# Kernel optimization log

Hardware: AMD Instinct MI355X
Metric: run time of the kernel (lower is better)

## Reference

```python
import jax, jax.numpy as jnp
import numpy as np

B, S, V, D, H, DH, L, FF = 1, 4096, 50265, 768, 12, 64, 4, 3072
C = 256          # chunk size
W = 256          # one-sided window (attention_window=512 total)
N = S // C


def _ln(x, g, b):
    m = x.mean(-1, keepdims=True)
    v = ((x - m) ** 2).mean(-1, keepdims=True)
    return (x - m) * jax.lax.rsqrt(v + 1e-5) * g + b


def setup_inputs() -> dict:
    key = jax.random.key(0)
    ks = iter(jax.random.split(key, 64))
    f = lambda sh: 0.02 * jax.random.normal(next(ks), sh, jnp.float32)
    return dict(
        input_ids=jax.random.randint(next(ks), (B, S), 0, V),
        attention_mask=jnp.ones((B, S), jnp.int32),
        word_emb=f((V, D)), pos_emb=f((S, D)),
        emb_g=jnp.ones((D,)), emb_b=jnp.zeros((D,)),
        Wq=f((L, D, D)), Wk=f((L, D, D)), Wv=f((L, D, D)), Wo=f((L, D, D)),
        bq=jnp.zeros((L, D)), bk=jnp.zeros((L, D)), bv=jnp.zeros((L, D)), bo=jnp.zeros((L, D)),
        ln1_g=jnp.ones((L, D)), ln1_b=jnp.zeros((L, D)),
        Wff1=f((L, D, FF)), bff1=jnp.zeros((L, FF)),
        Wff2=f((L, FF, D)), bff2=jnp.zeros((L, D)),
        ln2_g=jnp.ones((L, D)), ln2_b=jnp.zeros((L, D)),
        W1=f((D, 512)), b1=jnp.zeros((512,)),
        W2=f((512, 250)), b2=jnp.zeros((250,)),
        W3=f((250, 1)), b3=jnp.zeros((1,)),
    )


def _band_attn(x, maskf, Wq, Wk, Wv, Wo, bq, bk, bv, bo):
    # sliding-window (banded) attention via overlapping 3-chunk blocks
    q = ((x @ Wq + bq) / np.float32(np.sqrt(DH))).reshape(B, N, C, H, DH)
    k = (x @ Wk + bk).reshape(B, N, C, H, DH)
    v = (x @ Wv + bv).reshape(B, N, C, H, DH)
    pad = ((0, 0), (1, 1), (0, 0), (0, 0), (0, 0))
    kp, vp = jnp.pad(k, pad), jnp.pad(v, pad)
    kb = jnp.concatenate([kp[:, :-2], kp[:, 1:-1], kp[:, 2:]], axis=2)  # [B,N,3C,H,DH]
    vb = jnp.concatenate([vp[:, :-2], vp[:, 1:-1], vp[:, 2:]], axis=2)
    mc = maskf.reshape(B, N, C)
    mp = jnp.pad(mc, ((0, 0), (1, 1), (0, 0)))
    mb = jnp.concatenate([mp[:, :-2], mp[:, 1:-1], mp[:, 2:]], axis=2)  # [B,N,3C]
    qi = jnp.arange(C)[:, None]
    kj = jnp.arange(3 * C)[None, :]
    band = jnp.abs(kj - C - qi) <= W                       # [C,3C]
    valid = band[None, None, None] & (mb[:, None, :, None, :] > 0)  # [B,1,N,C,3C]
    scores = jnp.einsum('bnqhd,bnkhd->bhnqk', q, kb)       # [B,H,N,C,3C]
    scores = jnp.where(valid, scores, -1e9)
    probs = jax.nn.softmax(scores, axis=-1)
    out = jnp.einsum('bhnqk,bnkhd->bnqhd', probs, vb).reshape(B, S, D)
    return out @ Wo + bo


def reference(input_ids, attention_mask, word_emb, pos_emb, emb_g, emb_b,
              Wq, Wk, Wv, Wo, bq, bk, bv, bo, ln1_g, ln1_b,
              Wff1, bff1, Wff2, bff2, ln2_g, ln2_b,
              W1, b1, W2, b2, W3, b3):
    maskf = attention_mask.astype(jnp.float32)
    x = _ln(word_emb[input_ids] + pos_emb[None], emb_g, emb_b)
    for l in range(L):
        a = _band_attn(x, maskf, Wq[l], Wk[l], Wv[l], Wo[l], bq[l], bk[l], bv[l], bo[l])
        x = _ln(x + a, ln1_g[l], ln1_b[l])
        h = jax.nn.gelu(x @ Wff1[l] + bff1[l], approximate=False)
        x = _ln(x + h @ Wff2[l] + bff2[l], ln2_g[l], ln2_b[l])
    m = maskf[..., None]
    pooled = (x * m).sum(1) / jnp.clip(m.sum(1), 1e-9)     # mean pooling, [B,D]
    h = jax.nn.relu(pooled @ W1 + b1)
    h = jax.nn.relu(h @ W2 + b2)
    pred = h @ W3 + b3                                     # dropout = identity (eval)
    return (pred, pred)
```

## Files before the change

### kernel.cpp

```cpp
#include <hip/hip_runtime.h>
#include <hip/hip_bf16.h>

typedef __hip_bfloat16 bf16;
typedef unsigned short ushort_t;
typedef short bhalf8 __attribute__((ext_vector_type(8)));
typedef float floatx4 __attribute__((ext_vector_type(4)));

#define SLEN 4096
#define DMODEL 768
#define NHEAD 12
#define DHEAD 64
#define NLAYER 4
#define FFDIM 3072
#define WIN 256
#define QB 64
#define NKT 9
#define VT_PLANE (NHEAD*DHEAD*SLEN)

__device__ __forceinline__ float wave_sum(float v){
  #pragma unroll
  for (int off = 32; off; off >>= 1) v += __shfl_xor(v, off, 64);
  return v;
}

__device__ __forceinline__ ushort_t f2bf(float x){
  unsigned u = __float_as_uint(x);
  unsigned r = u + 0x7FFFu + ((u >> 16) & 1u);
  return (ushort_t)(r >> 16);
}
__device__ __forceinline__ float bf2f(ushort_t h){
  return __uint_as_float((unsigned)h << 16);
}

__device__ __forceinline__ floatx4 mfma_bf16(bhalf8 a, bhalf8 b, floatx4 c){
  asm("v_mfma_f32_16x16x32_bf16 %0, %1, %2, %0" : "+v"(c) : "v"(a), "v"(b));
  return c;
}

__device__ __forceinline__ void split8(const float* xs, bhalf8& hi, bhalf8& lo){
  union { ushort_t u[8]; bhalf8 v; } H, L;
  #pragma unroll
  for (int j = 0; j < 8; j++){
    ushort_t h = f2bf(xs[j]);
    H.u[j] = h;
    L.u[j] = f2bf(xs[j] - bf2f(h));
  }
  hi = H.v; lo = L.v;
}

__global__ __launch_bounds__(256) void embed_ln_kernel(
    const int* __restrict__ ids, const float* __restrict__ we,
    const float* __restrict__ pe, const float* __restrict__ g,
    const float* __restrict__ b, float* __restrict__ x){
  int row  = blockIdx.x*4 + (threadIdx.x >> 6);
  int lane = threadIdx.x & 63;
  int id = ids[row];
  float e[12];
  float sum = 0.f;
  #pragma unroll
  for (int i = 0; i < 12; i++){
    int c = lane + i*64;
    e[i] = we[(size_t)id*DMODEL + c] + pe[(size_t)row*DMODEL + c];
    sum += e[i];
  }
  float mean = wave_sum(sum) * (1.f/DMODEL);
  float vs = 0.f;
  #pragma unroll
  for (int i = 0; i < 12; i++){ float d = e[i] - mean; vs += d*d; }
  float inv = 1.f / sqrtf(wave_sum(vs)*(1.f/DMODEL) + 1e-5f);
  #pragma unroll
  for (int i = 0; i < 12; i++){
    int c = lane + i*64;
    x[(size_t)row*DMODEL + c] = (e[i] - mean)*inv*g[c] + b[c];
  }
}

__global__ __launch_bounds__(256) void ln_kernel(
    const float* __restrict__ in, float* __restrict__ out,
    const float* __restrict__ g, const float* __restrict__ b){
  int row  = blockIdx.x*4 + (threadIdx.x >> 6);
  int lane = threadIdx.x & 63;
  float e[12];
  float sum = 0.f;
  #pragma unroll
  for (int i = 0; i < 12; i++){
    e[i] = in[(size_t)row*DMODEL + lane + i*64];
    sum += e[i];
  }
  float mean = wave_sum(sum) * (1.f/DMODEL);
  float vs = 0.f;
  #pragma unroll
  for (int i = 0; i < 12; i++){ float d = e[i] - mean; vs += d*d; }
  float inv = 1.f / sqrtf(wave_sum(vs)*(1.f/DMODEL) + 1e-5f);
  #pragma unroll
  for (int i = 0; i < 12; i++){
    int c = lane + i*64;
    out[(size_t)row*DMODEL + c] = (e[i] - mean)*inv*g[c] + b[c];
  }
}

__global__ __launch_bounds__(256) void split_a_kernel(
    const float* __restrict__ X, ushort_t* __restrict__ T, int K){
  int idx = blockIdx.x*256 + threadIdx.x;
  int m  = idx & 4095;
  int kc = idx >> 12;
  const float* src = X + (size_t)m*K + kc*8;
  float4 x0 = *reinterpret_cast<const float4*>(src);
  float4 x1 = *reinterpret_cast<const float4*>(src + 4);
  float xs[8] = {x0.x,x0.y,x0.z,x0.w,x1.x,x1.y,x1.z,x1.w};
  union { ushort_t u[8]; uint4 v; } ph, pl;
  #pragma unroll
  for (int j = 0; j < 8; j++){
    ushort_t h = f2bf(xs[j]);
    ph.u[j] = h;
    pl.u[j] = f2bf(xs[j] - bf2f(h));
  }
  size_t KC = (size_t)(K >> 3);
  *reinterpret_cast<uint4*>(T + ((size_t)kc*4096 + m)*8)      = ph.v;
  *reinterpret_cast<uint4*>(T + ((KC + kc)*4096 + m)*8)       = pl.v;
}

__global__ __launch_bounds__(256) void split_b_kernel(
    const float* __restrict__ W, ushort_t* __restrict__ T, int N, int K){
  int n  = blockIdx.x*256 + threadIdx.x;
  int kc = blockIdx.y;
  float xs[8];
  #pragma unroll
  for (int j = 0; j < 8; j++) xs[j] = W[(size_t)(kc*8 + j)*N + n];
  union { ushort_t u[8]; uint4 v; } ph, pl;
  #pragma unroll
  for (int j = 0; j < 8; j++){
    ushort_t h = f2bf(xs[j]);
    ph.u[j] = h;
    pl.u[j] = f2bf(xs[j] - bf2f(h));
  }
  size_t KC = (size_t)(K >> 3);
  *reinterpret_cast<uint4*>(T + ((size_t)kc*N + n)*8)   = ph.v;
  *reinterpret_cast<uint4*>(T + ((KC + kc)*N + n)*8)    = pl.v;
}

__global__ __launch_bounds__(256) void gemm_mfma_kernel(
    const ushort_t* __restrict__ pAt,
    const ushort_t* __restrict__ pBt,
    const float* __restrict__ bias, const float* __restrict__ resid,
    float* __restrict__ Cm, int M, int N, int K, float scale, int act,
    ushort_t* __restrict__ vt_out){
  __shared__ __align__(16) ushort_t LAh[4][128][8];
  __shared__ __align__(16) ushort_t LAl[4][128][8];
  __shared__ __align__(16) ushort_t LBh[4][128][8];
  __shared__ __align__(16) ushort_t LBl[4][128][8];
  const int tid  = threadIdx.x;
  const int w    = tid >> 6;
  const int lane = tid & 63;
  const int wr = w >> 1, wc = w & 1;
  const int r0 = blockIdx.y*128, c0 = blockIdx.x*128;
  const int fr = lane & 15, fq = lane >> 4;
  const size_t KC = (size_t)(K >> 3);

  size_t plane; int rb; const ushort_t* gbase; ushort_t* lbase;
  if (w < 2){ plane = (size_t)M*8; rb = r0; } else { plane = (size_t)N*8; rb = c0; }
  if      (w == 0){ gbase = pAt;             lbase = &LAh[0][0][0]; }
  else if (w == 1){ gbase = pAt + KC*plane;  lbase = &LAl[0][0][0]; }
  else if (w == 2){ gbase = pBt;             lbase = &LBh[0][0][0]; }
  else            { gbase = pBt + KC*plane;  lbase = &LBl[0][0][0]; }

  floatx4 acc[4][4] = {};

  const int nstep = K >> 5;
  for (int s = 0; s < nstep; ++s){
    const int kcb = s << 2;
    #pragma unroll
    for (int ci = 0; ci < 8; ci++){
      const int kg = ci >> 1, half = ci & 1;
      const ushort_t* sp = gbase + (size_t)(kcb + kg)*plane
                         + (size_t)(rb + half*64 + lane)*8;
      ushort_t* dp = lbase + kg*1024 + half*512;
      __builtin_amdgcn_global_load_lds(
          (const __attribute__((address_space(1))) void*)sp,
          (__attribute__((address_space(3))) void*)dp, 16, 0, 0);
    }
    asm volatile("s_waitcnt vmcnt(0)" ::: "memory");
    __syncthreads();

    bhalf8 ah[4], al[4], bh[4], bl[4];
    #pragma unroll
    for (int mi = 0; mi < 4; mi++){
      int row = wr*64 + mi*16 + fr;
      ah[mi] = *reinterpret_cast<const bhalf8*>(&LAh[fq][row][0]);
      al[mi] = *reinterpret_cast<const bhalf8*>(&LAl[fq][row][0]);
    }
    #pragma unroll
    for (int ni = 0; ni < 4; ni++){
      int col = wc*64 + ni*16 + fr;
      bh[ni] = *reinterpret_cast<const bhalf8*>(&LBh[fq][col][0]);
      bl[ni] = *reinterpret_cast<const bhalf8*>(&LBl[fq][col][0]);
    }
    #pragma unroll
    for (int mi = 0; mi < 4; mi++)
      #pragma unroll
      for (int ni = 0; ni < 4; ni++)
        acc[mi][ni] = mfma_bf16(ah[mi], bh[ni], acc[mi][ni]);
    #pragma unroll
    for (int mi = 0; mi < 4; mi++)
      #pragma unroll
      for (int ni = 0; ni < 4; ni++)
        acc[mi][ni] = mfma_bf16(ah[mi], bl[ni], acc[mi][ni]);
    #pragma unroll
    for (int mi = 0; mi < 4; mi++)
      #pragma unroll
      for (int ni = 0; ni < 4; ni++)
        acc[mi][ni] = mfma_bf16(al[mi], bh[ni], acc[mi][ni]);
    __syncthreads();
  }

  if (vt_out){
    #pragma unroll
    for (int mi = 0; mi < 4; mi++){
      #pragma unroll
      for (int ni = 0; ni < 4; ni++){
        int col = c0 + wc*64 + ni*16 + fr;
        float bb = bias[col];
        int row0 = r0 + wr*64 + mi*16 + fq*4;
        unsigned long long phi = 0ull, plo = 0ull;
        #pragma unroll
        for (int j = 0; j < 4; j++){
          float vo = (acc[mi][ni][j] + bb) * scale;
          ushort_t hh = f2bf(vo);
          ushort_t ll = f2bf(vo - bf2f(hh));
          phi |= (unsigned long long)hh << (16*j);
          plo |= (unsigned long long)ll << (16*j);
        }
        size_t base = (size_t)col*SLEN + row0;
        *reinterpret_cast<unsigned long long*>(&vt_out[base])            = phi;
        *reinterpret_cast<unsigned long long*>(&vt_out[VT_PLANE + base]) = plo;
      }
    }
    return;
  }

  #pragma unroll
  for (int mi = 0; mi < 4; mi++){
    #pragma unroll
    for (int ni = 0; ni < 4; ni++){
      int col = c0 + wc*64 + ni*16 + fr;
      float bb = bias[col];
      #pragma unroll
      for (int j = 0; j < 4; j++){
        int row = r0 + wr*64 + mi*16 + fq*4 + j;
        float vo = (acc[mi][ni][j] + bb) * scale;
        if (act == 1) vo = 0.5f*vo*(1.f + erff(vo*0.70710678118654752f));
        if (resid) vo += resid[(size_t)row*N + col];
        Cm[(size_t)row*N + col] = vo;
      }
    }
  }
}

__global__ __launch_bounds__(128) void band_attn_kernel(
    const float* __restrict__ q, const float* __restrict__ k,
    const ushort_t* __restrict__ vt, const int* __restrict__ mask,
    float* __restrict__ ao){
  __shared__ __align__(16) ushort_t KHs[8][65][8];
  __shared__ __align__(16) ushort_t KLs[8][65][8];
  __shared__ __align__(16) ushort_t VHs[8][65][8];
  __shared__ __align__(16) ushort_t VLs[8][65][8];
  __shared__ __align__(16) ushort_t PHs[2][8][33][8];
  __shared__ __align__(16) ushort_t PLs[2][8][33][8];
  __shared__ float aL[2][32];
  __shared__ float lL[2][32];

  const int h    = blockIdx.y;
  const int q0   = blockIdx.x * QB;
  const int tid  = threadIdx.x;
  const int w    = tid >> 6;
  const int lane = tid & 63;
  const int fr   = lane & 15;
  const int fq   = lane >> 4;
  const int kstart = q0 - WIN;

  bhalf8 QHr[2][2], QLr[2][2];
  #pragma unroll
  for (int cf = 0; cf < 2; cf++)
    #pragma unroll
    for (int s = 0; s < 2; s++){
      const float* qp = q + (size_t)(q0 + 32*w + 16*cf + fr)*DMODEL
                      + h*DHEAD + s*32 + fq*8;
      float4 a = *reinterpret_cast<const float4*>(qp);
      float4 b = *reinterpret_cast<const float4*>(qp + 4);
      float xs[8] = {a.x,a.y,a.z,a.w,b.x,b.y,b.z,b.w};
      split8(xs, QHr[cf][s], QLr[cf][s]);
    }

  floatx4 acc_o[2][4] = {};
  float mreg[2] = {0.f, 0.f};
  float lreg[2] = {0.f, 0.f};

  const int rK = 32*w + (lane >> 1);
  const int hd = lane & 1;

  for (int t = 0; t < NKT; t++){
    const int g0 = kstart + t*64;

    {
      int g = min(max(g0 + rK, 0), SLEN-1);
      const float* kp = k + (size_t)g*DMODEL + h*DHEAD + hd*32;
      #pragma unroll
      for (int i = 0; i < 4; i++){
        float4 a = *reinterpret_cast<const float4*>(kp + i*8);
        float4 b = *reinterpret_cast<const float4*>(kp + i*8 + 4);
        float xs[8] = {a.x,a.y,a.z,a.w,b.x,b.y,b.z,b.w};
        bhalf8 hi, lo; split8(xs, hi, lo);
        int kg = hd*4 + i;
        *reinterpret_cast<bhalf8*>(&KHs[kg][rK][0]) = hi;
        *reinterpret_cast<bhalf8*>(&KLs[kg][rK][0]) = lo;
      }
      const ushort_t* vrow = vt + (size_t)(h*DHEAD + rK)*SLEN;
      #pragma unroll
      for (int i = 0; i < 4; i++){
        int kk = min(max(g0 + hd*32 + i*8, 0), SLEN-8);
        uint4 hv = *reinterpret_cast<const uint4*>(&vrow[kk]);
        uint4 lv = *reinterpret_cast<const uint4*>(&vrow[VT_PLANE + kk]);
        int u = hd*4 + i;
        *reinterpret_cast<uint4*>(&VHs[u][rK][0]) = hv;
        *reinterpret_cast<uint4*>(&VLs[u][rK][0]) = lv;
      }
    }
    __syncthreads();

    int gmk = g0 + lane;
    bool kvv = ((unsigned)gmk < (unsigned)SLEN) &&
               (mask[min(max(gmk,0),SLEN-1)] != 0);
    unsigned long long bal = __ballot(kvv);

    floatx4 acc_s[4][2] = {};
    #pragma unroll
    for (int s = 0; s < 2; s++)
      #pragma unroll
      for (int kf = 0; kf < 4; kf++){
        int row = 16*kf + fr;
        int kg  = s*4 + fq;
        bhalf8 KHf = *reinterpret_cast<const bhalf8*>(&KHs[kg][row][0]);
        bhalf8 KLf = *reinterpret_cast<const bhalf8*>(&KLs[kg][row][0]);
        #pragma unroll
        for (int cf = 0; cf < 2; cf++){
          acc_s[kf][cf] = mfma_bf16(KHf, QHr[cf][s], acc_s[kf][cf]);
          acc_s[kf][cf] = mfma_bf16(KHf, QLr[cf][s], acc_s[kf][cf]);
          acc_s[kf][cf] = mfma_bf16(KLf, QHr[cf][s], acc_s[kf][cf]);
        }
      }

    #pragma unroll
    for (int cf = 0; cf < 2; cf++){
      int qloc = 32*w + 16*cf + fr;
      float mx = -1e30f;
      #pragma unroll
      for (int kf = 0; kf < 4; kf++)
        #pragma unroll
        for (int j = 0; j < 4; j++){
          int key = 16*kf + fq*4 + j;
          int dj  = t*64 + key - WIN - qloc;
          bool ok = ((unsigned)(dj + WIN) <= 2u*WIN) && ((bal >> key) & 1ull);
          float sv = ok ? acc_s[kf][cf][j] : -1e30f;
          acc_s[kf][cf][j] = sv;
          mx = fmaxf(mx, sv);
        }
      mx = fmaxf(mx, __shfl_xor(mx, 16, 64));
      mx = fmaxf(mx, __shfl_xor(mx, 32, 64));
      float mnew  = fmaxf(mreg[cf], mx);
      float alpha = __expf(mreg[cf] - mnew);
      mreg[cf] = mnew;
      float psum = 0.f;
      #pragma unroll
      for (int kf = 0; kf < 4; kf++){
        unsigned long long phi = 0ull, plo = 0ull;
        #pragma unroll
        for (int j = 0; j < 4; j++){
          float p = __expf(acc_s[kf][cf][j] - mnew);
          psum += p;
          ushort_t hh = f2bf(p);
          ushort_t ll = f2bf(p - bf2f(hh));
          phi |= (unsigned long long)hh << (16*j);
          plo |= (unsigned long long)ll << (16*j);
        }
        int kgrp = 2*kf + (fq >> 1);
        int qrow = 16*cf + fr;
        *reinterpret_cast<unsigned long long*>(&PHs[w][kgrp][qrow][(fq&1)*4]) = phi;
        *reinterpret_cast<unsigned long long*>(&PLs[w][kgrp][qrow][(fq&1)*4]) = plo;
      }
      psum += __shfl_xor(psum, 16, 64);
      psum += __shfl_xor(psum, 32, 64);
      lreg[cf] = lreg[cf]*alpha + psum;
      if (fq == 0) aL[w][16*cf + fr] = alpha;
    }
    __syncthreads();

    #pragma unroll
    for (int mf = 0; mf < 2; mf++)
      #pragma unroll
      for (int j = 0; j < 4; j++){
        float al = aL[w][16*mf + fq*4 + j];
        #pragma unroll
        for (int ni = 0; ni < 4; ni++)
          acc_o[mf][ni][j] *= al;
      }

    #pragma unroll
    for (int ks = 0; ks < 2; ks++){
      int u = ks*4 + fq;
      bhalf8 PHf[2], PLf[2];
      #pragma unroll
      for (int mf = 0; mf < 2; mf++){
        PHf[mf] = *reinterpret_cast<const bhalf8*>(&PHs[w][u][16*mf + fr][0]);
        PLf[mf] = *reinterpret_cast<const bhalf8*>(&PLs[w][u][16*mf + fr][0]);
      }
      #pragma unroll
      for (int ni = 0; ni < 4; ni++){
        int d = 16*ni + fr;
        bhalf8 VHf = *reinterpret_cast<const bhalf8*>(&VHs[u][d][0]);
        bhalf8 VLf = *reinterpret_cast<const bhalf8*>(&VLs[u][d][0]);
        #pragma unroll
        for (int mf = 0; mf < 2; mf++){
          acc_o[mf][ni] = mfma_bf16(PHf[mf], VHf, acc_o[mf][ni]);
          acc_o[mf][ni] = mfma_bf16(PHf[mf], VLf, acc_o[mf][ni]);
          acc_o[mf][ni] = mfma_bf16(PLf[mf], VHf, acc_o[mf][ni]);
        }
      }
    }
    __syncthreads();
  }

  if (fq == 0){
    lL[w][fr]      = 1.f / lreg[0];
    lL[w][16 + fr] = 1.f / lreg[1];
  }
  __syncthreads();
  #pragma unroll
  for (int mf = 0; mf < 2; mf++)
    #pragma unroll
    for (int j = 0; j < 4; j++){
      float inv = lL[w][16*mf + fq*4 + j];
      int qg = q0 + 32*w + 16*mf + fq*4 + j;
      float* orow = ao + (size_t)qg*DMODEL + h*DHEAD;
      #pragma unroll
      for (int ni = 0; ni < 4; ni++)
        orow[16*ni + fr] = acc_o[mf][ni][j] * inv;
    }
}

__global__ __launch_bounds__(256) void pool1_kernel(
    const float* __restrict__ x, const int* __restrict__ mask,
    float* __restrict__ partial){
  int b = blockIdx.x;
  int t = threadIdx.x;
  float a0 = 0.f, a1 = 0.f, a2 = 0.f;
  for (int r = b*16; r < b*16 + 16; r++){
    float mm = (float)mask[r];
    const float* row = x + (size_t)r*DMODEL;
    a0 = fmaf(row[t      ], mm, a0);
    a1 = fmaf(row[t + 256], mm, a1);
    a2 = fmaf(row[t + 512], mm, a2);
  }
  partial[(size_t)b*DMODEL + t      ] = a0;
  partial[(size_t)b*DMODEL + t + 256] = a1;
  partial[(size_t)b*DMODEL + t + 512] = a2;
}

__global__ __launch_bounds__(256) void pool2_kernel(
    const float* __restrict__ partial, float* __restrict__ ps){
  int c = blockIdx.x*256 + threadIdx.x;
  float a = 0.f;
  for (int p = 0; p < 256; p++) a += partial[(size_t)p*DMODEL + c];
  ps[c] = a;
}

__global__ __launch_bounds__(64) void probe_kernel(
    const float* __restrict__ p, int n, float* __restrict__ slot){
  int lane = threadIdx.x;
  float s = 0.f;
  for (int i = lane; i < n; i += 64) s += fabsf(p[i]);
  s = wave_sum(s);
  if (lane == 0) slot[0] = s;
}

__global__ __launch_bounds__(256) void head_kernel(
    const float* __restrict__ ps, const int* __restrict__ mask,
    const float* __restrict__ W1, const float* __restrict__ b1,
    const float* __restrict__ W2, const float* __restrict__ b2,
    const float* __restrict__ W3, const float* __restrict__ b3,
    const float* __restrict__ diag,
    bf16* __restrict__ out){
  __shared__ float p[DMODEL];
  __shared__ float h1[512];
  __shared__ float h2[256];
  __shared__ float red[4];
  int tid = threadIdx.x;
  float ms = 0.f;
  for (int r = tid; r < SLEN; r += 256) ms += (float)mask[r];
  ms = wave_sum(ms);
  if ((tid & 63) == 0) red[tid >> 6] = ms;
  __syncthreads();
  float msum = red[0] + red[1] + red[2] + red[3];
  float inv = 1.f / fmaxf(msum, 1e-9f);
  for (int c = tid; c < DMODEL; c += 256) p[c] = ps[c]*inv;
  __syncthreads();
  #pragma unroll
  for (int jj = 0; jj < 2; jj++){
    int j = tid + jj*256;
    float acc = 0.f;
    for (int c = 0; c < DMODEL; c++) acc = fmaf(p[c], W1[(size_t)c*512 + j], acc);
    h1[j] = fmaxf(acc + b1[j], 0.f);
  }
  __syncthreads();
  if (tid < 250){
    float acc = 0.f;
    for (int c = 0; c < 512; c++) acc = fmaf(h1[c], W2[(size_t)c*250 + tid], acc);
    h2[tid] = fmaxf(acc + b2[tid], 0.f);
  }
  __syncthreads();
  if (tid == 0){
    float acc = b3[0];
    for (int c = 0; c < 250; c++) acc = fmaf(h2[c], W3[c], acc);
    float delta = 0.f;
    #pragma unroll
    for (int kk = 0; kk < 6; kk++){
      float dv = diag[kk];
      if (!(dv > 1e-3f)){
        delta = (dv != dv ? 8192.0f : 0.0f) + 64.0f*(kk+1);
        break;
      }
    }
    float r = acc + delta;
    union { bf16 h; unsigned short u; } cv;
    cv.h = (bf16)r;
    unsigned int packed = ((unsigned int)cv.u << 16) | (unsigned int)cv.u;
    volatile unsigned int* o32 = (volatile unsigned int*)out;
    o32[0] = packed;
    o32[1] = packed;
  }
}

extern "C" void kernel_launch(void* const* d_in, const int* in_sizes, int n_in,
                              void* d_out, int out_size, void* d_ws, size_t ws_size,
                              hipStream_t stream) {
  const int*   ids  = (const int*)d_in[0];
  const int*   mask = (const int*)d_in[1];
  const float* we   = (const float*)d_in[2];
  const float* pe   = (const float*)d_in[3];
  const float* eg   = (const float*)d_in[4];
  const float* eb   = (const float*)d_in[5];
  const float* Wq   = (const float*)d_in[6];
  const float* Wk   = (const float*)d_in[7];
  const float* Wv   = (const float*)d_in[8];
  const float* Wo   = (const float*)d_in[9];
  const float* bq   = (const float*)d_in[10];
  const float* bk   = (const float*)d_in[11];
  const float* bv   = (const float*)d_in[12];
  const float* bo   = (const float*)d_in[13];
  const float* g1   = (const float*)d_in[14];
  const float* be1  = (const float*)d_in[15];
  const float* Wf1  = (const float*)d_in[16];
  const float* bf1  = (const float*)d_in[17];
  const float* Wf2  = (const float*)d_in[18];
  const float* bf2  = (const float*)d_in[19];
  const float* g2   = (const float*)d_in[20];
  const float* be2  = (const float*)d_in[21];
  const float* W1   = (const float*)d_in[22];
  const float* b1   = (const float*)d_in[23];
  const float* W2   = (const float*)d_in[24];
  const float* b2   = (const float*)d_in[25];
  const float* W3   = (const float*)d_in[26];
  const float* b3   = (const float*)d_in[27];

  const size_t SD = (size_t)SLEN*DMODEL;
  float* x  = (float*)d_ws;
  float* y  = x  + SD;
  float* q  = y  + SD;
  float* k  = q  + SD;
  float* v  = k  + SD;
  float* ao = v  + SD;
  float* hf = q;
  ushort_t* vt = (ushort_t*)v;
  float* ps      = ao + SD;
  float* partial = ps + 1024;
  float* diag    = partial + 256*DMODEL;
  ushort_t* At = (ushort_t*)(diag + 64);
  ushort_t* Bt = At + (size_t)2*(FFDIM/8)*4096*8;

  embed_ln_kernel<<<SLEN/4, 256, 0, stream>>>(ids, we, pe, eg, eb, x);
  probe_kernel<<<1, 64, 0, stream>>>(x, 4096, diag + 0);

  const float qscale = 0.125f;
  dim3 gProj(DMODEL/128, SLEN/128);
  dim3 gFF1 (FFDIM/128,  SLEN/128);
  dim3 sbD(DMODEL/256, DMODEL/8);
  dim3 sbF1(FFDIM/256, DMODEL/8);
  dim3 sbF2(DMODEL/256, FFDIM/8);

  for (int l = 0; l < NLAYER; l++){
    const float* wq  = Wq  + (size_t)l*DMODEL*DMODEL;
    const float* wk  = Wk  + (size_t)l*DMODEL*DMODEL;
    const float* wv  = Wv  + (size_t)l*DMODEL*DMODEL;
    const float* wo  = Wo  + (size_t)l*DMODEL*DMODEL;
    const float* wf1 = Wf1 + (size_t)l*DMODEL*FFDIM;
    const float* wf2 = Wf2 + (size_t)l*FFDIM*DMODEL;

    split_a_kernel<<<(DMODEL/8)*SLEN/256, 256, 0, stream>>>(x, At, DMODEL);
    split_b_kernel<<<sbD, 256, 0, stream>>>(wq, Bt, DMODEL, DMODEL);
    gemm_mfma_kernel<<<gProj, 256, 0, stream>>>(At, Bt, bq + l*DMODEL, nullptr, q,
                                                SLEN, DMODEL, DMODEL, qscale, 0, nullptr);
    split_b_kernel<<<sbD, 256, 0, stream>>>(wk, Bt, DMODEL, DMODEL);
    gemm_mfma_kernel<<<gProj, 256, 0, stream>>>(At, Bt, bk + l*DMODEL, nullptr, k,
                                                SLEN, DMODEL, DMODEL, 1.f, 0, nullptr);
    split_b_kernel<<<sbD, 256, 0, stream>>>(wv, Bt, DMODEL, DMODEL);
    gemm_mfma_kernel<<<gProj, 256, 0, stream>>>(At, Bt, bv + l*DMODEL, nullptr, nullptr,
                                                SLEN, DMODEL, DMODEL, 1.f, 0, vt);
    if (l == 0) probe_kernel<<<1, 64, 0, stream>>>(q, 4096, diag + 1);
    if (l == 0) probe_kernel<<<1, 64, 0, stream>>>((const float*)vt, 4096, diag + 2);

    band_attn_kernel<<<dim3(SLEN/QB, NHEAD), 128, 0, stream>>>(q, k, vt, mask, ao);
    if (l == 0) probe_kernel<<<1, 64, 0, stream>>>(ao, 4096, diag + 3);

    split_a_kernel<<<(DMODEL/8)*SLEN/256, 256, 0, stream>>>(ao, At, DMODEL);
    split_b_kernel<<<sbD, 256, 0, stream>>>(wo, Bt, DMODEL, DMODEL);
    gemm_mfma_kernel<<<gProj, 256, 0, stream>>>(At, Bt, bo + l*DMODEL, x, y,
                                                SLEN, DMODEL, DMODEL, 1.f, 0, nullptr);
    ln_kernel<<<SLEN/4, 256, 0, stream>>>(y, x, g1 + l*DMODEL, be1 + l*DMODEL);

    split_a_kernel<<<(DMODEL/8)*SLEN/256, 256, 0, stream>>>(x, At, DMODEL);
    split_b_kernel<<<sbF1, 256, 0, stream>>>(wf1, Bt, FFDIM, DMODEL);
    gemm_mfma_kernel<<<gFF1, 256, 0, stream>>>(At, Bt, bf1 + l*FFDIM, nullptr, hf,
                                               SLEN, FFDIM, DMODEL, 1.f, 1, nullptr);
    split_a_kernel<<<(FFDIM/8)*SLEN/256, 256, 0, stream>>>(hf, At, FFDIM);
    split_b_kernel<<<sbF2, 256, 0, stream>>>(wf2, Bt, DMODEL, FFDIM);
    gemm_mfma_kernel<<<gProj, 256, 0, stream>>>(At, Bt, bf2 + l*DMODEL, x, y,
                                               SLEN, DMODEL, FFDIM, 1.f, 0, nullptr);
    ln_kernel<<<SLEN/4, 256, 0, stream>>>(y, x, g2 + l*DMODEL, be2 + l*DMODEL);
  }
  probe_kernel<<<1, 64, 0, stream>>>(x, 4096, diag + 4);

  pool1_kernel<<<256, 256, 0, stream>>>(x, mask, partial);
  pool2_kernel<<<DMODEL/256, 256, 0, stream>>>(partial, ps);
  probe_kernel<<<1, 64, 0, stream>>>(ps, DMODEL, diag + 5);
  head_kernel<<<1, 256, 0, stream>>>(ps, mask, W1, b1, W2, b2, W3, b3, diag, (bf16*)d_out);
}
```

Measured before the change: 2.273 ms.

## Fuse activation bf16 split into GEMM, merge QKV GEMM, double-buffer LDS

The separate split_a pass is removed. The GEMM now loads fp32 activations directly and converts them to hi/lo bf16 into LDS itself. Q, K and V are computed by one GEMM over a concatenated weight matrix, with per-section epilogues. The main loop is double-buffered, prefetching the next K-step while MFMAs run, and the M tile shrinks to 64 rows for more blocks. This removes extra launches and global round-trips of split activations, at the cost of in-kernel conversion work and halved per-block reuse of B.

```diff
diff --git a/kernel.cpp b/kernel.cpp
--- a/kernel.cpp
+++ b/kernel.cpp
@@ -99,15 +99,14 @@
   }
 }
 
-__global__ __launch_bounds__(256) void split_a_kernel(
-    const float* __restrict__ X, ushort_t* __restrict__ T, int K){
-  int idx = blockIdx.x*256 + threadIdx.x;
-  int m  = idx & 4095;
-  int kc = idx >> 12;
-  const float* src = X + (size_t)m*K + kc*8;
-  float4 x0 = *reinterpret_cast<const float4*>(src);
-  float4 x1 = *reinterpret_cast<const float4*>(src + 4);
-  float xs[8] = {x0.x,x0.y,x0.z,x0.w,x1.x,x1.y,x1.z,x1.w};
+__global__ __launch_bounds__(256) void split_b_kernel(
+    const float* __restrict__ W, ushort_t* __restrict__ T,
+    int Nw, int Ntot, int K, int noff){
+  int n  = blockIdx.x*256 + threadIdx.x;
+  int kc = blockIdx.y;
+  float xs[8];
+  #pragma unroll
+  for (int j = 0; j < 8; j++) xs[j] = W[(size_t)(kc*8 + j)*Nw + n];
   union { ushort_t u[8]; uint4 v; } ph, pl;
   #pragma unroll
   for (int j = 0; j < 8; j++){
@@ -116,139 +115,169 @@
     pl.u[j] = f2bf(xs[j] - bf2f(h));
   }
   size_t KC = (size_t)(K >> 3);
-  *reinterpret_cast<uint4*>(T + ((size_t)kc*4096 + m)*8)      = ph.v;
-  *reinterpret_cast<uint4*>(T + ((KC + kc)*4096 + m)*8)       = pl.v;
-}
-
-__global__ __launch_bounds__(256) void split_b_kernel(
-    const float* __restrict__ W, ushort_t* __restrict__ T, int N, int K){
-  int n  = blockIdx.x*256 + threadIdx.x;
-  int kc = blockIdx.y;
-  float xs[8];
-  #pragma unroll
-  for (int j = 0; j < 8; j++) xs[j] = W[(size_t)(kc*8 + j)*N + n];
-  union { ushort_t u[8]; uint4 v; } ph, pl;
-  #pragma unroll
-  for (int j = 0; j < 8; j++){
-    ushort_t h = f2bf(xs[j]);
-    ph.u[j] = h;
-    pl.u[j] = f2bf(xs[j] - bf2f(h));
-  }
-  size_t KC = (size_t)(K >> 3);
-  *reinterpret_cast<uint4*>(T + ((size_t)kc*N + n)*8)   = ph.v;
-  *reinterpret_cast<uint4*>(T + ((KC + kc)*N + n)*8)    = pl.v;
+  *reinterpret_cast<uint4*>(T + ((size_t)kc*Ntot + noff + n)*8)        = ph.v;
+  *reinterpret_cast<uint4*>(T + ((KC + kc)*Ntot + noff + n)*8)         = pl.v;
 }
 
 __global__ __launch_bounds__(256) void gemm_mfma_kernel(
-    const ushort_t* __restrict__ pAt,
-    const ushort_t* __restrict__ pBt,
-    const float* __restrict__ bias, const float* __restrict__ resid,
-    float* __restrict__ Cm, int M, int N, int K, float scale, int act,
-    ushort_t* __restrict__ vt_out){
-  __shared__ __align__(16) ushort_t LAh[4][128][8];
-  __shared__ __align__(16) ushort_t LAl[4][128][8];
-  __shared__ __align__(16) ushort_t LBh[4][128][8];
-  __shared__ __align__(16) ushort_t LBl[4][128][8];
+    const float* __restrict__ Afp, const ushort_t* __restrict__ pBt,
+    const float* __restrict__ bias, const float* __restrict__ bias2,
+    const float* __restrict__ bias3, const float* __restrict__ resid,
+    float* __restrict__ Cm, float* __restrict__ k_out,
+    ushort_t* __restrict__ vt_out,
+    int M, int N, int K, float scale, int mode){
+  __shared__ __align__(16) ushort_t LA[2][2][4][64][8];
+  __shared__ __align__(16) ushort_t LB[2][2][4][128][8];
   const int tid  = threadIdx.x;
   const int w    = tid >> 6;
   const int lane = tid & 63;
   const int wr = w >> 1, wc = w & 1;
-  const int r0 = blockIdx.y*128, c0 = blockIdx.x*128;
+  const int r0 = blockIdx.y*64, c0 = blockIdx.x*128;
   const int fr = lane & 15, fq = lane >> 4;
   const size_t KC = (size_t)(K >> 3);
-
-  size_t plane; int rb; const ushort_t* gbase; ushort_t* lbase;
-  if (w < 2){ plane = (size_t)M*8; rb = r0; } else { plane = (size_t)N*8; rb = c0; }
-  if      (w == 0){ gbase = pAt;             lbase = &LAh[0][0][0]; }
-  else if (w == 1){ gbase = pAt + KC*plane;  lbase = &LAl[0][0][0]; }
-  else if (w == 2){ gbase = pBt;             lbase = &LBh[0][0][0]; }
-  else            { gbase = pBt + KC*plane;  lbase = &LBl[0][0][0]; }
-
-  floatx4 acc[4][4] = {};
-
+  const size_t planeB = (size_t)N*8;
+
+  const int arow = tid >> 2;
+  const int akg  = tid & 3;
+  const float* asrc = Afp + (size_t)(r0 + arow)*K + akg*8;
+
+  floatx4 acc[2][4] = {};
   const int nstep = K >> 5;
+
+  #pragma unroll
+  for (int c = 0; c < 4; c++){
+    int idx = w*4 + c;
+    int half = idx >> 3, kg = (idx & 7) >> 1, sub = idx & 1;
+    const ushort_t* sp = pBt + (size_t)half*KC*planeB + (size_t)kg*planeB
+                       + (size_t)(c0 + sub*64 + lane)*8;
+    ushort_t* dp = &LB[0][half][kg][sub*64][0];
+    __builtin_amdgcn_global_load_lds(
+        (const __attribute__((address_space(1))) void*)sp,
+        (__attribute__((address_space(3))) void*)dp, 16, 0, 0);
+  }
+  {
+    float4 a0 = *reinterpret_cast<const float4*>(asrc);
+    float4 a1 = *reinterpret_cast<const float4*>(asrc + 4);
+    asm volatile("s_waitcnt vmcnt(0)" ::: "memory");
+    float xs[8] = {a0.x,a0.y,a0.z,a0.w,a1.x,a1.y,a1.z,a1.w};
+    bhalf8 hi, lo; split8(xs, hi, lo);
+    *reinterpret_cast<bhalf8*>(&LA[0][0][akg][arow][0]) = hi;
+    *reinterpret_cast<bhalf8*>(&LA[0][1][akg][arow][0]) = lo;
+  }
+  __syncthreads();
+
+  int cur = 0;
   for (int s = 0; s < nstep; ++s){
-    const int kcb = s << 2;
-    #pragma unroll
-    for (int ci = 0; ci < 8; ci++){
-      const int kg = ci >> 1, half = ci & 1;
-      const ushort_t* sp = gbase + (size_t)(kcb + kg)*plane
-                         + (size_t)(rb + half*64 + lane)*8;
-      ushort_t* dp = lbase + kg*1024 + half*512;
-      __builtin_amdgcn_global_load_lds(
-          (const __attribute__((address_space(1))) void*)sp,
-          (__attribute__((address_space(3))) void*)dp, 16, 0, 0);
-    }
-    asm volatile("s_waitcnt vmcnt(0)" ::: "memory");
-    __syncthreads();
-
-    bhalf8 ah[4], al[4], bh[4], bl[4];
-    #pragma unroll
-    for (int mi = 0; mi < 4; mi++){
-      int row = wr*64 + mi*16 + fr;
-      ah[mi] = *reinterpret_cast<const bhalf8*>(&LAh[fq][row][0]);
-      al[mi] = *reinterpret_cast<const bhalf8*>(&LAl[fq][row][0]);
+    const bool pf = (s+1 < nstep);
+    float4 pa0, pa1;
+    if (pf){
+      const int kcb = (s+1) << 2;
+      #pragma unroll
+      for (int c = 0; c < 4; c++){
+        int idx = w*4 + c;
+        int half = idx >> 3, kg = (idx & 7) >> 1, sub = idx & 1;
+        const ushort_t* sp = pBt + (size_t)half*KC*planeB + (size_t)(kcb + kg)*planeB
+                           + (size_t)(c0 + sub*64 + lane)*8;
+        ushort_t* dp = &LB[cur^1][half][kg][sub*64][0];
+        __builtin_amdgcn_global_load_lds(
+            (const __attribute__((address_space(1))) void*)sp,
+            (__attribute__((address_space(3))) void*)dp, 16, 0, 0);
+      }
+      const float* p = asrc + (size_t)(s+1)*32;
+      pa0 = *reinterpret_cast<const float4*>(p);
+      pa1 = *reinterpret_cast<const float4*>(p + 4);
+    }
+
+    bhalf8 ah[2], al[2], bh[4], bl[4];
+    #pragma unroll
+    for (int mi = 0; mi < 2; mi++){
+      int row = wr*32 + mi*16 + fr;
+      ah[mi] = *reinterpret_cast<const bhalf8*>(&LA[cur][0][fq][row][0]);
+      al[mi] = *reinterpret_cast<const bhalf8*>(&LA[cur][1][fq][row][0]);
     }
     #pragma unroll
     for (int ni = 0; ni < 4; ni++){
       int col = wc*64 + ni*16 + fr;
-      bh[ni] = *reinterpret_cast<const bhalf8*>(&LBh[fq][col][0]);
-      bl[ni] = *reinterpret_cast<const bhalf8*>(&LBl[fq][col][0]);
-    }
-    #pragma unroll
-    for (int mi = 0; mi < 4; mi++)
+      bh[ni] = *reinterpret_cast<const bhalf8*>(&LB[cur][0][fq][col][0]);
+      bl[ni] = *reinterpret_cast<const bhalf8*>(&LB[cur][1][fq][col][0]);
+    }
+    #pragma unroll
+    for (int mi = 0; mi < 2; mi++)
       #pragma unroll
       for (int ni = 0; ni < 4; ni++)
         acc[mi][ni] = mfma_bf16(ah[mi], bh[ni], acc[mi][ni]);
     #pragma unroll
-    for (int mi = 0; mi < 4; mi++)
+    for (int mi = 0; mi < 2; mi++)
       #pragma unroll
       for (int ni = 0; ni < 4; ni++)
         acc[mi][ni] = mfma_bf16(ah[mi], bl[ni], acc[mi][ni]);
     #pragma unroll
-    for (int mi = 0; mi < 4; mi++)
+    for (int mi = 0; mi < 2; mi++)
       #pragma unroll
       for (int ni = 0; ni < 4; ni++)
         acc[mi][ni] = mfma_bf16(al[mi], bh[ni], acc[mi][ni]);
+
+    if (pf){
+      asm volatile("s_waitcnt vmcnt(0)" ::: "memory");
+      float xs[8] = {pa0.x,pa0.y,pa0.z,pa0.w,pa1.x,pa1.y,pa1.z,pa1.w};
+      bhalf8 hi, lo; split8(xs, hi, lo);
+      *reinterpret_cast<bhalf8*>(&LA[cur^1][0][akg][arow][0]) = hi;
+      *reinterpret_cast<bhalf8*>(&LA[cur^1][1][akg][arow][0]) = lo;
+    }
     __syncthreads();
-  }
-
-  if (vt_out){
-    #pragma unroll
-    for (int mi = 0; mi < 4; mi++){
+    cur ^= 1;
+  }
+
+  if (mode == 2){
+    const int sect = c0 / DMODEL;
+    const int coff = c0 - sect*DMODEL;
+    #pragma unroll
+    for (int mi = 0; mi < 2; mi++){
       #pragma unroll
       for (int ni = 0; ni < 4; ni++){
-        int col = c0 + wc*64 + ni*16 + fr;
-        float bb = bias[col];
-        int row0 = r0 + wr*64 + mi*16 + fq*4;
-        unsigned long long phi = 0ull, plo = 0ull;
-        #pragma unroll
-        for (int j = 0; j < 4; j++){
-          float vo = (acc[mi][ni][j] + bb) * scale;
-          ushort_t hh = f2bf(vo);
-          ushort_t ll = f2bf(vo - bf2f(hh));
-          phi |= (unsigned long long)hh << (16*j);
-          plo |= (unsigned long long)ll << (16*j);
+        int col = coff + wc*64 + ni*16 + fr;
+        int row0 = r0 + wr*32 + mi*16 + fq*4;
+        if (sect == 0){
+          float bb = bias[col];
+          #pragma unroll
+          for (int j = 0; j < 4; j++)
+            Cm[(size_t)(row0+j)*DMODEL + col] = (acc[mi][ni][j] + bb) * scale;
+        } else if (sect == 1){
+          float bb = bias2[col];
+          #pragma unroll
+          for (int j = 0; j < 4; j++)
+            k_out[(size_t)(row0+j)*DMODEL + col] = acc[mi][ni][j] + bb;
+        } else {
+          float bb = bias3[col];
+          unsigned long long phi = 0ull, plo = 0ull;
+          #pragma unroll
+          for (int j = 0; j < 4; j++){
+            float vo = acc[mi][ni][j] + bb;
+            ushort_t hh = f2bf(vo);
+            ushort_t ll = f2bf(vo - bf2f(hh));
+            phi |= (unsigned long long)hh << (16*j);
+            plo |= (unsigned long long)ll << (16*j);
+          }
+          size_t base = (size_t)col*SLEN + row0;
+          *reinterpret_cast<unsigned long long*>(&vt_out[base])            = phi;
+          *reinterpret_cast<unsigned long long*>(&vt_out[VT_PLANE + base]) = plo;
         }
-        size_t base = (size_t)col*SLEN + row0;
-        *reinterpret_cast<unsigned long long*>(&vt_out[base])            = phi;
-        *reinterpret_cast<unsigned long long*>(&vt_out[VT_PLANE + base]) = plo;
       }
     }
     return;
   }
 
   #pragma unroll
-  for (int mi = 0; mi < 4; mi++){
+  for (int mi = 0; mi < 2; mi++){
     #pragma unroll
     for (int ni = 0; ni < 4; ni++){
       int col = c0 + wc*64 + ni*16 + fr;
       float bb = bias[col];
       #pragma unroll
       for (int j = 0; j < 4; j++){
-        int row = r0 + wr*64 + mi*16 + fq*4 + j;
+        int row = r0 + wr*32 + mi*16 + fq*4 + j;
         float vo = (acc[mi][ni][j] + bb) * scale;
-        if (act == 1) vo = 0.5f*vo*(1.f + erff(vo*0.70710678118654752f));
+        if (mode == 1) vo = 0.5f*vo*(1.f + erff(vo*0.70710678118654752f));
         if (resid) vo += resid[(size_t)row*N + col];
         Cm[(size_t)row*N + col] = vo;
       }
@@ -583,18 +612,15 @@
   float* ps      = ao + SD;
   float* partial = ps + 1024;
   float* diag    = partial + 256*DMODEL;
-  ushort_t* At = (ushort_t*)(diag + 64);
-  ushort_t* Bt = At + (size_t)2*(FFDIM/8)*4096*8;
+  ushort_t* Bt = (ushort_t*)(diag + 64);
 
   embed_ln_kernel<<<SLEN/4, 256, 0, stream>>>(ids, we, pe, eg, eb, x);
   probe_kernel<<<1, 64, 0, stream>>>(x, 4096, diag + 0);
 
   const float qscale = 0.125f;
-  dim3 gProj(DMODEL/128, SLEN/128);
-  dim3 gFF1 (FFDIM/128,  SLEN/128);
-  dim3 sbD(DMODEL/256, DMODEL/8);
-  dim3 sbF1(FFDIM/256, DMODEL/8);
-  dim3 sbF2(DMODEL/256, FFDIM/8);
+  dim3 gQKV((DMODEL*3)/128, SLEN/64);
+  dim3 gD  (DMODEL/128,     SLEN/64);
+  dim3 gF1 (FFDIM/128,      SLEN/64);
 
   for (int l = 0; l < NLAYER; l++){
     const float* wq  = Wq  + (size_t)l*DMODEL*DMODEL;
@@ -604,36 +630,33 @@
     const float* wf1 = Wf1 + (size_t)l*DMODEL*FFDIM;
     const float* wf2 = Wf2 + (size_t)l*FFDIM*DMODEL;
 
-    split_a_kernel<<<(DMODEL/8)*SLEN/256, 256, 0, stream>>>(x, At, DMODEL);
-    split_b_kernel<<<sbD, 256, 0, stream>>>(wq, Bt, DMODEL, DMODEL);
-    gemm_mfma_kernel<<<gProj, 256, 0, stream>>>(At, Bt, bq + l*DMODEL, nullptr, q,
-                                                SLEN, DMODEL, DMODEL, qscale, 0, nullptr);
-    split_b_kernel<<<sbD, 256, 0, stream>>>(wk, Bt, DMODEL, DMODEL);
-    gemm_mfma_kernel<<<gProj, 256, 0, stream>>>(At, Bt, bk + l*DMODEL, nullptr, k,
-                                                SLEN, DMODEL, DMODEL, 1.f, 0, nullptr);
-    split_b_kernel<<<sbD, 256, 0, stream>>>(wv, Bt, DMODEL, DMODEL);
-    gemm_mfma_kernel<<<gProj, 256, 0, stream>>>(At, Bt, bv + l*DMODEL, nullptr, nullptr,
-                                                SLEN, DMODEL, DMODEL, 1.f, 0, vt);
+    split_b_kernel<<<dim3(3,96), 256, 0, stream>>>(wq, Bt, DMODEL, 3*DMODEL, DMODEL, 0);
+    split_b_kernel<<<dim3(3,96), 256, 0, stream>>>(wk, Bt, DMODEL, 3*DMODEL, DMODEL, DMODEL);
+    split_b_kernel<<<dim3(3,96), 256, 0, stream>>>(wv, Bt, DMODEL, 3*DMODEL, DMODEL, 2*DMODEL);
+    gemm_mfma_kernel<<<gQKV, 256, 0, stream>>>(
+        x, Bt, bq + l*DMODEL, bk + l*DMODEL, bv + l*DMODEL, nullptr,
+        q, k, vt, SLEN, 3*DMODEL, DMODEL, qscale, 2);
     if (l == 0) probe_kernel<<<1, 64, 0, stream>>>(q, 4096, diag + 1);
     if (l == 0) probe_kernel<<<1, 64, 0, stream>>>((const float*)vt, 4096, diag + 2);
 
     band_attn_kernel<<<dim3(SLEN/QB, NHEAD), 128, 0, stream>>>(q, k, vt, mask, ao);
     if (l == 0) probe_kernel<<<1, 64, 0, stream>>>(ao, 4096, diag + 3);
 
-    split_a_kernel<<<(DMODEL/8)*SLEN/256, 256, 0, stream>>>(ao, At, DMODEL);
-    split_b_kernel<<<sbD, 256, 0, stream>>>(wo, Bt, DMODEL, DMODEL);
-    gemm_mfma_kernel<<<gProj, 256, 0, stream>>>(At, Bt, bo + l*DMODEL, x, y,
-                                                SLEN, DMODEL, DMODEL, 1.f, 0, nullptr);
+    split_b_kernel<<<dim3(3,96), 256, 0, stream>>>(wo, Bt, DMODEL, DMODEL, DMODEL, 0);
+    gemm_mfma_kernel<<<gD, 256, 0, stream>>>(
+        ao, Bt, bo + l*DMODEL, nullptr, nullptr, x,
+        y, nullptr, nullptr, SLEN, DMODEL, DMODEL, 1.f, 0);
     ln_kernel<<<SLEN/4, 256, 0, stream>>>(y, x, g1 + l*DMODEL, be1 + l*DMODEL);
 
-    split_a_kernel<<<(DMODEL/8)*SLEN/256, 256, 0, stream>>>(x, At, DMODEL);
-    split_b_kernel<<<sbF1, 256, 0, stream>>>(wf1, Bt, FFDIM, DMODEL);
-    gemm_mfma_kernel<<<gFF1, 256, 0, stream>>>(At, Bt, bf1 + l*FFDIM, nullptr, hf,
-                                               SLEN, FFDIM, DMODEL, 1.f, 1, nullptr);
-    split_a_kernel<<<(FFDIM/8)*SLEN/256, 256, 0, stream>>>(hf, At, FFDIM);
-    split_b_kernel<<<sbF2, 256, 0, stream>>>(wf2, Bt, DMODEL, FFDIM);
-    gemm_mfma_kernel<<<gProj, 256, 0, stream>>>(At, Bt, bf2 + l*DMODEL, x, y,
-                                               SLEN, DMODEL, FFDIM, 1.f, 0, nullptr);
+    split_b_kernel<<<dim3(12,96), 256, 0, stream>>>(wf1, Bt, FFDIM, FFDIM, DMODEL, 0);
+    gemm_mfma_kernel<<<gF1, 256, 0, stream>>>(
+        x, Bt, bf1 + l*FFDIM, nullptr, nullptr, nullptr,
+        hf, nullptr, nullptr, SLEN, FFDIM, DMODEL, 1.f, 1);
+
+    split_b_kernel<<<dim3(3,384), 256, 0, stream>>>(wf2, Bt, DMODEL, DMODEL, FFDIM, 0);
+    gemm_mfma_kernel<<<gD, 256, 0, stream>>>(
+        hf, Bt, bf2 + l*DMODEL, nullptr, nullptr, x,
+        y, nullptr, nullptr, SLEN, DMODEL, FFDIM, 1.f, 0);
     ln_kernel<<<SLEN/4, 256, 0, stream>>>(y, x, g2 + l*DMODEL, be2 + l*DMODEL);
   }
   probe_kernel<<<1, 64, 0, stream>>>(x, 4096, diag + 4);
```

Result: faster. 2.067 ms (-9.0%).
